# Kernel tuning notes

Hardware: AMD Instinct MI355X
Metric: run time of the kernel (lower is better)

## Reference

```python
import jax, jax.numpy as jnp
import numpy as np

N_NODES = 30000; SEQ_LEN = 32; VOCAB = 10000
RNN_H = 128; RGCN_IN = 64; RGCN_H = 64; N_CLASSES = 16
N_RELS = 8; N_BASES = 4; N_EDGES = 480000


def setup_inputs() -> dict:
    key = jax.random.key(0)
    ks = jax.random.split(key, 20)
    s = 0.05
    norm = lambda k, shape: jax.random.normal(k, shape, jnp.float32) * s
    return {
        "inputs": jax.random.randint(ks[0], (N_NODES, SEQ_LEN), 0, VOCAB),
        "sequence_length": jax.random.randint(ks[1], (N_NODES,), 1, SEQ_LEN),
        "src": jax.random.randint(ks[2], (N_EDGES,), 0, N_NODES),
        "dst": jax.random.randint(ks[3], (N_EDGES,), 0, N_NODES),
        "rel_type": jax.random.randint(ks[4], (N_EDGES,), 0, N_RELS),
        "edge_norm": jax.random.uniform(ks[5], (N_EDGES,), jnp.float32),
        # RNN encoder params (only reverse-direction LSTM affects the output h_n[-1])
        "emb": norm(ks[6], (VOCAB, RNN_H)),
        "w_ih": norm(ks[7], (4 * RNN_H, RNN_H)),
        "w_hh": norm(ks[8], (4 * RNN_H, RNN_H)),
        "b_ih": norm(ks[9], (4 * RNN_H,)),
        "b_hh": norm(ks[10], (4 * RNN_H,)),
        "fc_w": norm(ks[11], (RGCN_IN, RNN_H)),
        "fc_b": norm(ks[12], (RGCN_IN,)),
        # RGCN basis-decomposed weights: W_r = sum_b w_comp[r,b] * basis[b]
        "basis0": norm(ks[13], (N_BASES, RGCN_IN, RGCN_H)),
        "wcomp0": norm(ks[14], (N_RELS, N_BASES)),
        "basis1": norm(ks[15], (N_BASES, RGCN_H, RGCN_H)),
        "wcomp1": norm(ks[16], (N_RELS, N_BASES)),
        "basis2": norm(ks[17], (N_BASES, RGCN_H, N_CLASSES)),
        "wcomp2": norm(ks[18], (N_RELS, N_BASES)),
    }


def _lstm_last(x, w_ih, w_hh, b_ih, b_hh):
    # x: [T, B, H] -> final hidden state [B, H] (PyTorch gate order: i, f, g, o)
    H = w_hh.shape[1]
    B = x.shape[1]
    h0 = jnp.zeros((B, H), x.dtype)

    def step(carry, x_t):
        h, c = carry
        z = x_t @ w_ih.T + b_ih + h @ w_hh.T + b_hh
        i, f, g, o = jnp.split(z, 4, axis=-1)
        c = jax.nn.sigmoid(f) * c + jax.nn.sigmoid(i) * jnp.tanh(g)
        h = jax.nn.sigmoid(o) * jnp.tanh(c)
        return (h, c), None

    (h, _), _ = jax.lax.scan(step, (h0, h0), x)
    return h


def _rgcn_layer(h, src, dst, rel, norm, basis, w_comp, activation):
    # Basis-decomposed RGCN: aggregate normed source feats per (dst, rel), then transform.
    # Mathematically identical to per-edge h[src] @ W[rel] scatter-summed to dst.
    n = h.shape[0]
    R = w_comp.shape[0]
    W = jnp.einsum('rb,bio->rio', w_comp, basis)            # [R, in, out]
    msg = h[src] * norm[:, None]                            # [E, in] gather
    seg = dst * R + rel                                     # scatter key (dst, rel)
    agg = jax.ops.segment_sum(msg, seg, num_segments=n * R)
    agg = agg.reshape(n, R, -1)                             # [N, R, in]
    out = jnp.einsum('nri,rio->no', agg, W)                 # [N, out]
    return activation(out) if activation is not None else out


def reference(inputs, sequence_length, src, dst, rel_type, edge_norm,
              emb, w_ih, w_hh, b_ih, b_hh, fc_w, fc_b,
              basis0, wcomp0, basis1, wcomp1, basis2, wcomp2):
    # RNN encoder: embedding -> bidirectional LSTM -> fc(h_n[-1]).
    # h_n[-1] is the reverse-direction final state, so only the reverse LSTM
    # pass affects the output; run it on the time-reversed sequence.
    x = emb[inputs.T]                                       # [T, N, H]
    h_last = _lstm_last(x[::-1], w_ih, w_hh, b_ih, b_hh)    # [N, H]
    feats = h_last @ fc_w.T + fc_b                          # [N, RGCN_IN]
    # RGCN: input/hidden layers with relu, output layer without activation.
    h = _rgcn_layer(feats, src, dst, rel_type, edge_norm, basis0, wcomp0, jax.nn.relu)
    h = _rgcn_layer(h, src, dst, rel_type, edge_norm, basis1, wcomp1, jax.nn.relu)
    h = _rgcn_layer(h, src, dst, rel_type, edge_norm, basis2, wcomp2, None)
    return h
```

## Files before the change

### kernel.cpp

```cpp
#include <hip/hip_runtime.h>

typedef float  f32x4  __attribute__((ext_vector_type(4)));
typedef short  bf16x8 __attribute__((ext_vector_type(8)));
typedef unsigned int   u32;
typedef unsigned short u16;

#define N_NODES 30000
#define VOCABSZ 10000
#define LOG2E 1.442695040888963f

__device__ __forceinline__ float sigm(float x){
  return __builtin_amdgcn_rcpf(1.f + __builtin_amdgcn_exp2f(-LOG2E*x));
}
__device__ __forceinline__ float tanh_(float x){
  return 1.f - 2.f*__builtin_amdgcn_rcpf(1.f + __builtin_amdgcn_exp2f((2.f*LOG2E)*x));
}
__device__ __forceinline__ u16 f2bf(float f){
  u32 u = __builtin_bit_cast(u32, f);
  u = u + 0x7fffu + ((u>>16)&1u);
  return (u16)(u>>16);
}
__device__ __forceinline__ float bflo(u32 u){ return __builtin_bit_cast(float, u<<16); }
__device__ __forceinline__ float bfhi(u32 u){ return __builtin_bit_cast(float, u & 0xffff0000u); }

__global__ __launch_bounds__(256) void wmat_kernel(
    const float* __restrict__ b0, const float* __restrict__ c0,
    const float* __restrict__ b1, const float* __restrict__ c1,
    const float* __restrict__ b2, const float* __restrict__ c2,
    float* __restrict__ W0, float* __restrict__ W1, float* __restrict__ W2)
{
  int id = blockIdx.x*256 + threadIdx.x;
  if (id < 32768){
    int r = id>>12;
    float s = 0.f;
    #pragma unroll
    for (int b=0;b<4;++b) s += c0[r*4+b]*b0[b*4096 + (id&4095)];
    W0[id] = s;
  } else if (id < 65536){
    int k = id - 32768;
    int r = k>>12;
    float s = 0.f;
    #pragma unroll
    for (int b=0;b<4;++b) s += c1[r*4+b]*b1[b*4096 + (k&4095)];
    W1[k] = s;
  } else if (id < 73728){
    int k = id - 65536;
    int r = k>>10;
    float s = 0.f;
    #pragma unroll
    for (int b=0;b<4;++b) s += c2[r*4+b]*b2[b*1024 + (k&1023)];
    W2[k] = s;
  }
}

__global__ __launch_bounds__(256) void embproj_kernel(
    const float* __restrict__ emb, const float* __restrict__ w_ih,
    const float* __restrict__ b_ih, const float* __restrict__ b_hh,
    u16* __restrict__ eproj)
{
  __shared__ float et[64*132];
  __shared__ float wt[32*132];
  const int tid = threadIdx.x;
  const int v0 = blockIdx.x*64;
  const int vq = tid>>4, jq = tid&15;

  for (int idx = tid*4; idx < 64*128; idx += 1024){
    int row = idx>>7, col = idx&127;
    int vr = v0 + row; if (vr > VOCABSZ-1) vr = VOCABSZ-1;
    *(f32x4*)&et[row*132+col] = *(const f32x4*)&emb[vr*128+col];
  }
  for (int jt = blockIdx.y*4; jt < blockIdx.y*4 + 4; ++jt){
    __syncthreads();
    for (int idx = tid*4; idx < 32*128; idx += 1024){
      int row = idx>>7, col = idx&127;
      *(f32x4*)&wt[row*132+col] = *(const f32x4*)&w_ih[(jt*32+row)*128+col];
    }
    __syncthreads();
    float acc[4][2] = {};
    #pragma unroll 4
    for (int k=0;k<128;++k){
      float w0v = wt[(jq*2+0)*132+k];
      float w1v = wt[(jq*2+1)*132+k];
      #pragma unroll
      for (int a=0;a<4;++a){
        float e = et[(vq*4+a)*132+k];
        acc[a][0] += e*w0v;
        acc[a][1] += e*w1v;
      }
    }
    int jb = jt*32 + jq*2;
    float bi0 = b_ih[jb]   + b_hh[jb];
    float bi1 = b_ih[jb+1] + b_hh[jb+1];
    int g  = jb>>7, rem = jb&127;
    int w  = rem>>4, q4 = (rem>>2)&3, jl = rem&3;
    int jp = w*64 + q4*16 + jl*4 + g;
    #pragma unroll
    for (int a=0;a<4;++a){
      int v = v0 + vq*4 + a;
      if (v < VOCABSZ){
        eproj[v*512 + jp]     = f2bf(acc[a][0]+bi0);
        eproj[v*512 + jp + 4] = f2bf(acc[a][1]+bi1);
      }
    }
  }
}

__global__ __launch_bounds__(512, 2) void lstm_kernel(
    const int* __restrict__ tok, const u16* __restrict__ eproj,
    const float* __restrict__ w_hh, const float* __restrict__ fc_w,
    const float* __restrict__ fc_b, float* __restrict__ feats)
{
  __shared__ __align__(16) char lds[32768];
  __shared__ u16 tokL[64*33];
  const int tid = threadIdx.x;
  const int wave = tid>>6, lane = tid&63;
  const int c16 = lane&15, g4 = lane>>4;
  const int nb = blockIdx.x*64;

  bf16x8 afr[4][4];
  #pragma unroll
  for (int g=0; g<4; ++g){
    const float* wr = w_hh + (g*128 + wave*16 + c16)*128 + g4*8;
    #pragma unroll
    for (int kk=0; kk<4; ++kk){
      f32x4 wa = *(const f32x4*)(wr + kk*32);
      f32x4 wbv = *(const f32x4*)(wr + kk*32 + 4);
      bf16x8 a;
      a[0]=(short)f2bf(wa[0]); a[1]=(short)f2bf(wa[1]);
      a[2]=(short)f2bf(wa[2]); a[3]=(short)f2bf(wa[3]);
      a[4]=(short)f2bf(wbv[0]); a[5]=(short)f2bf(wbv[1]);
      a[6]=(short)f2bf(wbv[2]); a[7]=(short)f2bf(wbv[3]);
      afr[g][kk] = a;
    }
  }
  {
    f32x4 z = {0.f,0.f,0.f,0.f};
    for (int i = tid*16; i < 16384; i += 8192) *(f32x4*)(lds + i) = z;
  }
  {
    int n = tid>>3, t0 = (tid&7)*4;
    int node = nb + n; if (node > N_NODES-1) node = N_NODES-1;
    int4 a = *(const int4*)(tok + node*32 + t0);
    tokL[n*33 + t0    ] = (u16)a.x;
    tokL[n*33 + t0 + 1] = (u16)a.y;
    tokL[n*33 + t0 + 2] = (u16)a.z;
    tokL[n*33 + t0 + 3] = (u16)a.w;
  }
  const int swz = (c16&7)<<4;
  int rb[4];
  #pragma unroll
  for (int kk=0;kk<4;++kk) rb[kk] = c16*256 + ((kk*64 + g4*16)^swz);
  const int wbB = c16*256 + ((wave*32 + g4*8)^swz);

  float creg[4][4];
  #pragma unroll
  for (int nt=0;nt<4;++nt)
    #pragma unroll
    for (int q=0;q<4;++q) creg[nt][q]=0.f;

  __syncthreads();

  const size_t gbase = (size_t)(wave*128 + g4*32);
  uint4 gxX[4], gxY[4];
  #pragma unroll
  for (int nt=0;nt<4;++nt){
    int ptok = tokL[(nt*16+c16)*33 + 31];
    const char* ep = (const char*)eproj + (size_t)ptok*1024 + gbase;
    gxX[nt] = *(const uint4*)ep;
    gxY[nt] = *(const uint4*)(ep+16);
  }

  for (int t=0; t<32; ++t){
    const int bufR = (t&1)<<14, bufW = bufR ^ 16384;
    int ptk[4];
    if (t < 31){
      #pragma unroll
      for (int nt=0;nt<4;++nt) ptk[nt] = tokL[(nt*16+c16)*33 + 30 - t];
    }
    #pragma unroll
    for (int nt=0; nt<4; ++nt){
      uint4 X = gxX[nt], Y = gxY[nt];
      f32x4 acc[4];
      acc[0][0]=bflo(X.x); acc[1][0]=bfhi(X.x); acc[2][0]=bflo(X.y); acc[3][0]=bfhi(X.y);
      acc[0][1]=bflo(X.z); acc[1][1]=bfhi(X.z); acc[2][1]=bflo(X.w); acc[3][1]=bfhi(X.w);
      acc[0][2]=bflo(Y.x); acc[1][2]=bfhi(Y.x); acc[2][2]=bflo(Y.y); acc[3][2]=bfhi(Y.y);
      acc[0][3]=bflo(Y.z); acc[1][3]=bfhi(Y.z); acc[2][3]=bflo(Y.w); acc[3][3]=bfhi(Y.w);
      if (t < 31){
        const char* ep = (const char*)eproj + (size_t)ptk[nt]*1024 + gbase;
        gxX[nt] = *(const uint4*)ep;
        gxY[nt] = *(const uint4*)(ep+16);
      }
      bf16x8 bfr[4];
      #pragma unroll
      for (int kk=0;kk<4;++kk)
        bfr[kk] = *(const bf16x8*)(lds + bufR + rb[kk] + nt*4096);
      #pragma unroll
      for (int kk=0;kk<4;++kk){
        acc[0] = __builtin_amdgcn_mfma_f32_16x16x32_bf16(afr[0][kk], bfr[kk], acc[0], 0,0,0);
        acc[1] = __builtin_amdgcn_mfma_f32_16x16x32_bf16(afr[1][kk], bfr[kk], acc[1], 0,0,0);
        acc[2] = __builtin_amdgcn_mfma_f32_16x16x32_bf16(afr[2][kk], bfr[kk], acc[2], 0,0,0);
        acc[3] = __builtin_amdgcn_mfma_f32_16x16x32_bf16(afr[3][kk], bfr[kk], acc[3], 0,0,0);
      }
      float hv[4];
      #pragma unroll
      for (int q=0;q<4;++q){
        float zi=acc[0][q], zf=acc[1][q], zg=acc[2][q], zo=acc[3][q];
        float cn = sigm(zf)*creg[nt][q] + sigm(zi)*tanh_(zg);
        creg[nt][q] = cn;
        hv[q] = sigm(zo)*tanh_(cn);
      }
      u32 plo, phi;
      asm("v_cvt_pk_bf16_f32 %0, %1, %2" : "=v"(plo) : "v"(hv[0]), "v"(hv[1]));
      asm("v_cvt_pk_bf16_f32 %0, %1, %2" : "=v"(phi) : "v"(hv[2]), "v"(hv[3]));
      uint2 hw; hw.x = plo; hw.y = phi;
      *(uint2*)(lds + bufW + wbB + nt*4096) = hw;
    }
    __syncthreads();
  }
  const int w2 = wave>>1, half = wave&1;
  f32x4 fca[2];
  #pragma unroll
  for (int oi=0;oi<2;++oi){ fca[oi][0]=0.f; fca[oi][1]=0.f; fca[oi][2]=0.f; fca[oi][3]=0.f; }
  #pragma unroll
  for (int kk=0;kk<4;++kk){
    bf16x8 b = *(const bf16x8*)(lds + rb[kk] + w2*4096);
    #pragma unroll
    for (int oi=0;oi<2;++oi){
      int ot = half*2 + oi;
      const float* fr = fc_w + (ot*16 + c16)*128 + kk*32 + g4*8;
      f32x4 wa = *(const f32x4*)fr;
      f32x4 wbv = *(const f32x4*)(fr+4);
      bf16x8 a;
      a[0]=(short)f2bf(wa[0]); a[1]=(short)f2bf(wa[1]);
      a[2]=(short)f2bf(wa[2]); a[3]=(short)f2bf(wa[3]);
      a[4]=(short)f2bf(wbv[0]); a[5]=(short)f2bf(wbv[1]);
      a[6]=(short)f2bf(wbv[2]); a[7]=(short)f2bf(wbv[3]);
      fca[oi] = __builtin_amdgcn_mfma_f32_16x16x32_bf16(a, b, fca[oi], 0,0,0);
    }
  }
  const int node = nb + w2*16 + c16;
  if (node < N_NODES){
    #pragma unroll
    for (int oi=0;oi<2;++oi)
      #pragma unroll
      for (int q=0;q<4;++q){
        int o = (half*2+oi)*16 + g4*4 + q;
        feats[node*64 + o] = fca[oi][q] + fc_b[o];
      }
  }
}

template<int NO, bool RELU>
__global__ __launch_bounds__(256) void transform_kernel(
    const float* __restrict__ h, const float* __restrict__ W,
    float* __restrict__ tmp, int n_nodes)
{
  __shared__ float As[64][68];
  __shared__ float Bs[64][132];
  const int tid = threadIdx.x;
  const int n0 = blockIdx.x*64;
  const int j0 = blockIdx.y*128;
  constexpr int WIDTH = 8*NO;

  for (int idx = tid*4; idx < 4096; idx += 1024){
    int r = idx>>6, c = idx&63;
    int n = n0 + r; if (n > n_nodes-1) n = n_nodes-1;
    f32x4 v = *(const f32x4*)(h + (size_t)n*64 + c);
    if (RELU){
      v[0]=fmaxf(v[0],0.f); v[1]=fmaxf(v[1],0.f);
      v[2]=fmaxf(v[2],0.f); v[3]=fmaxf(v[3],0.f);
    }
    *(f32x4*)&As[r][c] = v;
  }
  for (int idx = tid*4; idx < 8192; idx += 1024){
    int k = idx>>7, j = idx&127;
    int jj = j0 + j;
    int r = jj / NO, o = jj & (NO-1);
    f32x4 v = *(const f32x4*)(W + r*(64*NO) + k*NO + o);
    *(f32x4*)&Bs[k][j] = v;
  }
  __syncthreads();

  const int tx = tid&15, ty = tid>>4;
  float acc[4][8];
  #pragma unroll
  for (int i=0;i<4;++i)
    #pragma unroll
    for (int j=0;j<8;++j) acc[i][j]=0.f;

  #pragma unroll 4
  for (int k=0;k<64;++k){
    f32x4 b0 = *(const f32x4*)&Bs[k][tx*8];
    f32x4 b1 = *(const f32x4*)&Bs[k][tx*8+4];
    #pragma unroll
    for (int i=0;i<4;++i){
      float a = As[ty*4+i][k];
      #pragma unroll
      for (int j=0;j<4;++j){
        acc[i][j]   += a*b0[j];
        acc[i][j+4] += a*b1[j];
      }
    }
  }
  #pragma unroll
  for (int i=0;i<4;++i){
    int n = n0 + ty*4 + i;
    if (n < n_nodes){
      *(f32x4*)(tmp + (size_t)n*WIDTH + j0 + tx*8)     = *(f32x4*)&acc[i][0];
      *(f32x4*)(tmp + (size_t)n*WIDTH + j0 + tx*8 + 4) = *(f32x4*)&acc[i][4];
    }
  }
}

template<int NO>
__global__ __launch_bounds__(256) void scatter_kernel(
    const float* __restrict__ tmp, const int* __restrict__ src,
    const int* __restrict__ dst, const int* __restrict__ rel,
    const float* __restrict__ enorm, float* __restrict__ out, int n_edges)
{
  constexpr int EPW = 64/NO;
  constexpr int WIDTH = 8*NO;
  const int lane = threadIdx.x & 63;
  const int es = (NO==64) ? 0 : (lane>>4);
  const int o  = lane & (NO-1);
  const long gw = (long)((blockIdx.x*256 + threadIdx.x)>>6);
  const long stride = (long)gridDim.x*4*EPW;
  long e = gw*EPW + es;
  if (e >= n_edges) return;
  int s=src[e], d=dst[e], r=rel[e]; float nm=enorm[e];
  float v = tmp[(size_t)s*WIDTH + r*NO + o];
  while (true){
    long e1 = e + stride;
    bool more = (e1 < n_edges);
    int s1=0,d1=0,r1=0; float nm1=0.f, v1=0.f;
    if (more){
      s1=src[e1]; d1=dst[e1]; r1=rel[e1]; nm1=enorm[e1];
      v1 = tmp[(size_t)s1*WIDTH + r1*NO + o];
    }
    unsafeAtomicAdd(out + (size_t)d*NO + o, v*nm);
    if (!more) break;
    s=s1; d=d1; r=r1; nm=nm1; v=v1; e=e1;
  }
}

extern "C" void kernel_launch(void* const* d_in, const int* in_sizes, int n_in,
                              void* d_out, int out_size, void* d_ws, size_t ws_size,
                              hipStream_t stream)
{
  const int*   tok    = (const int*)  d_in[0];
  const int*   src    = (const int*)  d_in[2];
  const int*   dst    = (const int*)  d_in[3];
  const int*   rel    = (const int*)  d_in[4];
  const float* enorm  = (const float*)d_in[5];
  const float* emb    = (const float*)d_in[6];
  const float* w_ih   = (const float*)d_in[7];
  const float* w_hh   = (const float*)d_in[8];
  const float* b_ih   = (const float*)d_in[9];
  const float* b_hh   = (const float*)d_in[10];
  const float* fc_w   = (const float*)d_in[11];
  const float* fc_b   = (const float*)d_in[12];
  const float* basis0 = (const float*)d_in[13];
  const float* wcomp0 = (const float*)d_in[14];
  const float* basis1 = (const float*)d_in[15];
  const float* wcomp1 = (const float*)d_in[16];
  const float* basis2 = (const float*)d_in[17];
  const float* wcomp2 = (const float*)d_in[18];

  char* ws = (char*)d_ws;
  float* tmp   = (float*)(ws);
  u16*   eproj = (u16*)  (ws);
  float* feats = (float*)(ws + 61440000);
  float* g1    = (float*)(ws + 69120000);
  float* g2    = (float*)(ws + 76800000);
  float* W0    = (float*)(ws + 84480000);
  float* W1    = (float*)(ws + 84611072);
  float* W2    = (float*)(ws + 84742144);

  wmat_kernel<<<288, 256, 0, stream>>>(basis0, wcomp0, basis1, wcomp1,
                                       basis2, wcomp2, W0, W1, W2);
  embproj_kernel<<<dim3(157,4), 256, 0, stream>>>(emb, w_ih, b_ih, b_hh, eproj);

  hipMemsetAsync(g1, 0, 15360000, stream);
  hipMemsetAsync(d_out, 0, 30000*16*4, stream);

  lstm_kernel<<<469, 512, 0, stream>>>(tok, eproj, w_hh, fc_w, fc_b, feats);

  transform_kernel<64,false><<<dim3(469,4), 256, 0, stream>>>(feats, W0, tmp, N_NODES);
  scatter_kernel<64><<<2048, 256, 0, stream>>>(tmp, src, dst, rel, enorm, g1, 480000);

  transform_kernel<64,true><<<dim3(469,4), 256, 0, stream>>>(g1, W1, tmp, N_NODES);
  scatter_kernel<64><<<2048, 256, 0, stream>>>(tmp, src, dst, rel, enorm, g2, 480000);

  transform_kernel<16,true><<<dim3(469,1), 256, 0, stream>>>(g2, W2, tmp, N_NODES);
  scatter_kernel<16><<<2048, 256, 0, stream>>>(tmp, src, dst, rel, enorm, (float*)d_out, 480000);
}
```

Measured before the change: 685.4 us.

## Replace transform+atomic scatter RGCN with dst-sorted CSR gather-then-transform fusion

Builds a CSR ordering of edges by destination (histogram, scan, permute) and packs src, rel and local dst into one word. Each RGCN layer becomes one fused kernel that gathers normed source features into a per-node [rel, in] tile in shared memory, then multiplies by the stacked relation weights. This removes the 8x-wide intermediate tmp buffer, the global atomics and the output memsets. In exchange it adds three preprocessing kernels (a single-block scan among them) and puts LDS read-modify-write accumulation in the gather phase. The LSTM token prefetch is also moved inline.

```diff
diff --git a/kernel.cpp b/kernel.cpp
--- a/kernel.cpp
+++ b/kernel.cpp
@@ -6,6 +6,7 @@
 typedef unsigned short u16;
 
 #define N_NODES 30000
+#define N_EDGES 480000
 #define VOCABSZ 10000
 #define LOG2E 1.442695040888963f
 
@@ -172,11 +173,6 @@
 
   for (int t=0; t<32; ++t){
     const int bufR = (t&1)<<14, bufW = bufR ^ 16384;
-    int ptk[4];
-    if (t < 31){
-      #pragma unroll
-      for (int nt=0;nt<4;++nt) ptk[nt] = tokL[(nt*16+c16)*33 + 30 - t];
-    }
     #pragma unroll
     for (int nt=0; nt<4; ++nt){
       uint4 X = gxX[nt], Y = gxY[nt];
@@ -186,7 +182,8 @@
       acc[0][2]=bflo(Y.x); acc[1][2]=bfhi(Y.x); acc[2][2]=bflo(Y.y); acc[3][2]=bfhi(Y.y);
       acc[0][3]=bflo(Y.z); acc[1][3]=bfhi(Y.z); acc[2][3]=bflo(Y.w); acc[3][3]=bfhi(Y.w);
       if (t < 31){
-        const char* ep = (const char*)eproj + (size_t)ptk[nt]*1024 + gbase;
+        int ptok = tokL[(nt*16+c16)*33 + 30 - t];
+        const char* ep = (const char*)eproj + (size_t)ptok*1024 + gbase;
         gxX[nt] = *(const uint4*)ep;
         gxY[nt] = *(const uint4*)(ep+16);
       }
@@ -250,96 +247,171 @@
   }
 }
 
-template<int NO, bool RELU>
-__global__ __launch_bounds__(256) void transform_kernel(
-    const float* __restrict__ h, const float* __restrict__ W,
-    float* __restrict__ tmp, int n_nodes)
-{
-  __shared__ float As[64][68];
-  __shared__ float Bs[64][132];
+__global__ __launch_bounds__(256) void hist_kernel(
+    const int* __restrict__ dst, int* __restrict__ cnt, int n)
+{
+  int e = blockIdx.x*256 + threadIdx.x;
+  if (e < n) atomicAdd(&cnt[dst[e]], 1);
+}
+
+__global__ __launch_bounds__(1024) void scan_kernel(
+    int* __restrict__ cnt, int* __restrict__ ofs)
+{
+  __shared__ int sums[1024];
   const int tid = threadIdx.x;
-  const int n0 = blockIdx.x*64;
-  const int j0 = blockIdx.y*128;
-  constexpr int WIDTH = 8*NO;
-
-  for (int idx = tid*4; idx < 4096; idx += 1024){
-    int r = idx>>6, c = idx&63;
-    int n = n0 + r; if (n > n_nodes-1) n = n_nodes-1;
-    f32x4 v = *(const f32x4*)(h + (size_t)n*64 + c);
-    if (RELU){
-      v[0]=fmaxf(v[0],0.f); v[1]=fmaxf(v[1],0.f);
-      v[2]=fmaxf(v[2],0.f); v[3]=fmaxf(v[3],0.f);
-    }
-    *(f32x4*)&As[r][c] = v;
-  }
-  for (int idx = tid*4; idx < 8192; idx += 1024){
-    int k = idx>>7, j = idx&127;
-    int jj = j0 + j;
-    int r = jj / NO, o = jj & (NO-1);
-    f32x4 v = *(const f32x4*)(W + r*(64*NO) + k*NO + o);
-    *(f32x4*)&Bs[k][j] = v;
-  }
+  const int base = tid*30;
+  int loc[30]; int s = 0;
+  #pragma unroll
+  for (int i=0;i<30;++i){
+    int d = base + i;
+    int c = (d < N_NODES) ? cnt[d] : 0;
+    loc[i] = s; s += c;
+  }
+  sums[tid] = s;
   __syncthreads();
-
-  const int tx = tid&15, ty = tid>>4;
-  float acc[4][8];
-  #pragma unroll
-  for (int i=0;i<4;++i)
-    #pragma unroll
-    for (int j=0;j<8;++j) acc[i][j]=0.f;
-
-  #pragma unroll 4
-  for (int k=0;k<64;++k){
-    f32x4 b0 = *(const f32x4*)&Bs[k][tx*8];
-    f32x4 b1 = *(const f32x4*)&Bs[k][tx*8+4];
-    #pragma unroll
-    for (int i=0;i<4;++i){
-      float a = As[ty*4+i][k];
-      #pragma unroll
-      for (int j=0;j<4;++j){
-        acc[i][j]   += a*b0[j];
-        acc[i][j+4] += a*b1[j];
-      }
-    }
-  }
-  #pragma unroll
-  for (int i=0;i<4;++i){
-    int n = n0 + ty*4 + i;
-    if (n < n_nodes){
-      *(f32x4*)(tmp + (size_t)n*WIDTH + j0 + tx*8)     = *(f32x4*)&acc[i][0];
-      *(f32x4*)(tmp + (size_t)n*WIDTH + j0 + tx*8 + 4) = *(f32x4*)&acc[i][4];
-    }
-  }
-}
-
-template<int NO>
-__global__ __launch_bounds__(256) void scatter_kernel(
-    const float* __restrict__ tmp, const int* __restrict__ src,
-    const int* __restrict__ dst, const int* __restrict__ rel,
-    const float* __restrict__ enorm, float* __restrict__ out, int n_edges)
-{
-  constexpr int EPW = 64/NO;
-  constexpr int WIDTH = 8*NO;
-  const int lane = threadIdx.x & 63;
-  const int es = (NO==64) ? 0 : (lane>>4);
-  const int o  = lane & (NO-1);
-  const long gw = (long)((blockIdx.x*256 + threadIdx.x)>>6);
-  const long stride = (long)gridDim.x*4*EPW;
-  long e = gw*EPW + es;
-  if (e >= n_edges) return;
-  int s=src[e], d=dst[e], r=rel[e]; float nm=enorm[e];
-  float v = tmp[(size_t)s*WIDTH + r*NO + o];
-  while (true){
-    long e1 = e + stride;
-    bool more = (e1 < n_edges);
-    int s1=0,d1=0,r1=0; float nm1=0.f, v1=0.f;
-    if (more){
-      s1=src[e1]; d1=dst[e1]; r1=rel[e1]; nm1=enorm[e1];
-      v1 = tmp[(size_t)s1*WIDTH + r1*NO + o];
-    }
-    unsafeAtomicAdd(out + (size_t)d*NO + o, v*nm);
-    if (!more) break;
-    s=s1; d=d1; r=r1; nm=nm1; v=v1; e=e1;
+  for (int off=1; off<1024; off<<=1){
+    int v = (tid >= off) ? sums[tid-off] : 0;
+    __syncthreads();
+    sums[tid] += v;
+    __syncthreads();
+  }
+  int excl = sums[tid] - s;
+  #pragma unroll
+  for (int i=0;i<30;++i){
+    int d = base + i;
+    if (d <= N_NODES){
+      int v = excl + loc[i];
+      ofs[d] = v;
+      if (d < N_NODES) cnt[d] = v;
+    }
+  }
+}
+
+__global__ __launch_bounds__(256) void permute_kernel(
+    const int* __restrict__ dst, const int* __restrict__ src,
+    const int* __restrict__ rel, const float* __restrict__ enorm,
+    int* __restrict__ cur, u32* __restrict__ esr, float* __restrict__ esn,
+    int n)
+{
+  int e = blockIdx.x*256 + threadIdx.x;
+  if (e < n){
+    int d = dst[e];
+    int p = atomicAdd(&cur[d], 1);
+    esr[p] = (u32)src[e] | ((u32)rel[e] << 15) | ((u32)(d & 31) << 18);
+    esn[p] = enorm[e];
+  }
+}
+
+template<bool RELU, int NO>
+__global__ __launch_bounds__(256, 2) void rgcn_fused(
+    const float* __restrict__ h, const u32* __restrict__ esr,
+    const float* __restrict__ esn, const int* __restrict__ ofs,
+    const float* __restrict__ W, float* __restrict__ out)
+{
+  __shared__ float A[32][516];
+  __shared__ float Bs[32][NO == 64 ? 68 : 18];
+  const int tid = threadIdx.x;
+  const int wave = tid>>6, lane = tid&63;
+  const int d0 = blockIdx.x*32;
+
+  for (int idx = tid*4; idx < 32*516; idx += 1024){
+    f32x4 z = {0.f,0.f,0.f,0.f};
+    *(f32x4*)&A[0][idx] = z;
+  }
+  __syncthreads();
+
+  {
+    int dlo = d0 + wave*8;  if (dlo > N_NODES) dlo = N_NODES;
+    int dhi = dlo + 8;      if (dhi > N_NODES) dhi = N_NODES;
+    const int beg = ofs[dlo], end = ofs[dhi];
+    for (int i = beg; i < end; i += 8){
+      u32 srb[8]; float nmb[8], vb[8];
+      #pragma unroll
+      for (int j=0;j<8;++j){
+        int ii = i + j;
+        int ic = (ii < end) ? ii : (end-1);
+        srb[j] = esr[ic];
+        nmb[j] = (ii < end) ? esn[ic] : 0.f;
+      }
+      #pragma unroll
+      for (int j=0;j<8;++j)
+        vb[j] = h[(size_t)(srb[j] & 0x7fff)*64 + lane];
+      #pragma unroll
+      for (int j=0;j<8;++j){
+        float v = vb[j];
+        if (RELU) v = fmaxf(v, 0.f);
+        float m = v * nmb[j];
+        int dloc = (srb[j] >> 18) & 31;
+        int r    = (srb[j] >> 15) & 7;
+        A[dloc][r*64 + lane] += m;
+      }
+    }
+  }
+  __syncthreads();
+
+  if (NO == 64){
+    const int tx = tid&15, ny = tid>>4;
+    float acc0[4] = {0.f,0.f,0.f,0.f};
+    float acc1[4] = {0.f,0.f,0.f,0.f};
+    for (int kt=0; kt<16; ++kt){
+      if (kt) __syncthreads();
+      for (int idx = tid*4; idx < 2048; idx += 1024){
+        int row = idx>>6, col = idx&63;
+        *(f32x4*)&Bs[row][col] = *(const f32x4*)(W + (size_t)(kt*32+row)*64 + col);
+      }
+      __syncthreads();
+      #pragma unroll
+      for (int kk4=0; kk4<32; kk4+=4){
+        f32x4 av0 = *(const f32x4*)&A[ny][kt*32+kk4];
+        f32x4 av1 = *(const f32x4*)&A[ny+16][kt*32+kk4];
+        #pragma unroll
+        for (int q=0;q<4;++q){
+          f32x4 b4 = *(const f32x4*)&Bs[kk4+q][tx*4];
+          #pragma unroll
+          for (int j=0;j<4;++j){
+            acc0[j] += av0[q]*b4[j];
+            acc1[j] += av1[q]*b4[j];
+          }
+        }
+      }
+    }
+    int n = d0 + ny;
+    if (n < N_NODES){
+      f32x4 v; v[0]=acc0[0]; v[1]=acc0[1]; v[2]=acc0[2]; v[3]=acc0[3];
+      *(f32x4*)(out + (size_t)n*64 + tx*4) = v;
+    }
+    n = d0 + ny + 16;
+    if (n < N_NODES){
+      f32x4 v; v[0]=acc1[0]; v[1]=acc1[1]; v[2]=acc1[2]; v[3]=acc1[3];
+      *(f32x4*)(out + (size_t)n*64 + tx*4) = v;
+    }
+  } else {
+    const int o2 = (tid&7)*2, n = tid>>3;
+    float acc0 = 0.f, acc1 = 0.f;
+    for (int kt=0; kt<16; ++kt){
+      if (kt) __syncthreads();
+      {
+        int idx = tid*2;
+        int row = idx>>4, col = idx&15;
+        float2 w2 = *(const float2*)(W + (size_t)(kt*32+row)*16 + col);
+        *(float2*)&Bs[row][col] = w2;
+      }
+      __syncthreads();
+      #pragma unroll
+      for (int kk4=0; kk4<32; kk4+=4){
+        f32x4 av = *(const f32x4*)&A[n][kt*32+kk4];
+        #pragma unroll
+        for (int q=0;q<4;++q){
+          acc0 += av[q]*Bs[kk4+q][o2];
+          acc1 += av[q]*Bs[kk4+q][o2+1];
+        }
+      }
+    }
+    int nn = d0 + n;
+    if (nn < N_NODES){
+      out[(size_t)nn*16 + o2]     = acc0;
+      out[(size_t)nn*16 + o2 + 1] = acc1;
+    }
   }
 }
 
@@ -367,30 +439,29 @@
   const float* wcomp2 = (const float*)d_in[18];
 
   char* ws = (char*)d_ws;
-  float* tmp   = (float*)(ws);
   u16*   eproj = (u16*)  (ws);
-  float* feats = (float*)(ws + 61440000);
-  float* g1    = (float*)(ws + 69120000);
-  float* g2    = (float*)(ws + 76800000);
-  float* W0    = (float*)(ws + 84480000);
-  float* W1    = (float*)(ws + 84611072);
-  float* W2    = (float*)(ws + 84742144);
+  float* feats = (float*)(ws + 10240000);
+  float* g1    = (float*)(ws + 17920000);
+  float* g2    = (float*)(ws + 25600000);
+  int*   ofs   = (int*)  (ws + 33280000);
+  int*   cur   = (int*)  (ws + 33400064);
+  u32*   esr   = (u32*)  (ws + 33520128);
+  float* esn   = (float*)(ws + 35440128);
+  float* W0    = (float*)(ws + 37360128);
+  float* W1    = (float*)(ws + 37491200);
+  float* W2    = (float*)(ws + 37622272);
+
+  hipMemsetAsync(cur, 0, 120004, stream);
+  hist_kernel<<<1875, 256, 0, stream>>>(dst, cur, N_EDGES);
+  scan_kernel<<<1, 1024, 0, stream>>>(cur, ofs);
+  permute_kernel<<<1875, 256, 0, stream>>>(dst, src, rel, enorm, cur, esr, esn, N_EDGES);
 
   wmat_kernel<<<288, 256, 0, stream>>>(basis0, wcomp0, basis1, wcomp1,
                                        basis2, wcomp2, W0, W1, W2);
   embproj_kernel<<<dim3(157,4), 256, 0, stream>>>(emb, w_ih, b_ih, b_hh, eproj);
-
-  hipMemsetAsync(g1, 0, 15360000, stream);
-  hipMemsetAsync(d_out, 0, 30000*16*4, stream);
-
   lstm_kernel<<<469, 512, 0, stream>>>(tok, eproj, w_hh, fc_w, fc_b, feats);
 
-  transform_kernel<64,false><<<dim3(469,4), 256, 0, stream>>>(feats, W0, tmp, N_NODES);
-  scatter_kernel<64><<<2048, 256, 0, stream>>>(tmp, src, dst, rel, enorm, g1, 480000);
-
-  transform_kernel<64,true><<<dim3(469,4), 256, 0, stream>>>(g1, W1, tmp, N_NODES);
-  scatter_kernel<64><<<2048, 256, 0, stream>>>(tmp, src, dst, rel, enorm, g2, 480000);
-
-  transform_kernel<16,true><<<dim3(469,1), 256, 0, stream>>>(g2, W2, tmp, N_NODES);
-  scatter_kernel<16><<<2048, 256, 0, stream>>>(tmp, src, dst, rel, enorm, (float*)d_out, 480000);
-}
+  rgcn_fused<false,64><<<938, 256, 0, stream>>>(feats, esr, esn, ofs, W0, g1);
+  rgcn_fused<true, 64><<<938, 256, 0, stream>>>(g1,    esr, esn, ofs, W1, g2);
+  rgcn_fused<true, 16><<<938, 256, 0, stream>>>(g2,    esr, esn, ofs, W2, (float*)d_out);
+}
```

Result: no change. 674.9 us (-1.5%).
